# Kernel tuning notes

Hardware: AMD Instinct MI355X
Metric: run time of the kernel (lower is better)

Reference implementation:

```python
import jax, jax.numpy as jnp
import numpy as np
import math

N_EMBD = 1024
N_HEAD = 16
N_LAYER = 12


def setup_inputs() -> dict:
    key = jax.random.key(0)
    kx, kw, kb = jax.random.split(key, 3)
    B, T, C = 4, 2048, N_EMBD
    x = jax.random.normal(kx, (B, T, C), dtype=jnp.float32)
    # nn.Linear(C, 3C): weight [3C, C] scaled by 1/sqrt(2*n_layer), bias [3C]
    bound = 1.0 / math.sqrt(C)
    W = jax.random.uniform(kw, (3 * C, C), minval=-bound, maxval=bound, dtype=jnp.float32)
    W = W * (1.0 / math.sqrt(N_LAYER * 2))
    b = jax.random.uniform(kb, (3 * C,), minval=-bound, maxval=bound, dtype=jnp.float32)
    return {"x": x, "W": W, "b": b}


def reference(x, W, b) -> jnp.ndarray:
    B, T, C = x.shape
    H = N_HEAD
    D = C // H
    qkv = jnp.einsum("btc,oc->bto", x, W) + b  # [B, T, 3C]
    q, k, v = jnp.split(qkv, 3, axis=-1)
    # [B, H, T, D]
    q = q.reshape(B, T, H, D).transpose(0, 2, 1, 3)
    k = k.reshape(B, T, H, D).transpose(0, 2, 1, 3)
    v = v.reshape(B, T, H, D).transpose(0, 2, 1, 3)
    att = jnp.einsum("bhtd,bhsd->bhts", q, k) / math.sqrt(D)  # [B, H, T, T]
    causal = jnp.tril(jnp.ones((T, T), dtype=bool))
    att = jnp.where(causal, att, -jnp.inf)
    att = jax.nn.softmax(att, axis=-1)
    y = jnp.einsum("bhts,bhsd->bhtd", att, v)  # [B, H, T, D]
    return y.transpose(0, 2, 1, 3).reshape(B, T, C)
```

## Files before the change

kernel.cpp:

```cpp
#include <hip/hip_runtime.h>


typedef __attribute__((ext_vector_type(8))) short short8;
typedef __attribute__((ext_vector_type(4))) float f32x4;
typedef __attribute__((ext_vector_type(2))) int int2v;

#define AS1 __attribute__((address_space(1)))
#define AS3 __attribute__((address_space(3)))

__device__ __forceinline__ unsigned short f2bf(float f) {
  unsigned int u = __float_as_uint(f);
  u += 0x7fffu + ((u >> 16) & 1u);
  return (unsigned short)(u >> 16);
}

__device__ __forceinline__ unsigned int pack_bf16(float lo, float hi) {
  return __builtin_amdgcn_perm(__float_as_uint(hi) + 0x8000u,
                               __float_as_uint(lo) + 0x8000u, 0x07060302u);
}

__device__ __forceinline__ void async_copy16(const unsigned short* g, unsigned short* l) {
  const AS1 unsigned char* gp = (const AS1 unsigned char*)(unsigned long long)(uintptr_t)g;
  AS3 unsigned char* lp = (AS3 unsigned char*)(unsigned int)(uintptr_t)l;
  __builtin_amdgcn_global_load_lds((const AS1 void*)gp, (AS3 void*)lp, 16, 0, 0);
}

__global__ __launch_bounds__(256) void cvt_both(const float* __restrict__ x,
                                                const float* __restrict__ W,
                                                unsigned short* __restrict__ xt,
                                                unsigned short* __restrict__ wt) {
  int U = blockIdx.x * 256 + threadIdx.x;
  const float* in;
  unsigned short* out;
  if (U < 1048576) { in = x; out = xt; }
  else             { in = W; out = wt; U -= 1048576; }
  int u6 = U & 63, frag = (U >> 6) & 15, kt = (U >> 10) & 15, bt = U >> 14;
  int ks = frag & 1, i = (frag >> 1) & 3, half = frag >> 3;
  int row = bt * 128 + half * 64 + i * 16 + (u6 & 15);
  int colf = kt * 64 + ks * 32 + (u6 >> 4) * 8;
  const float4* p = (const float4*)(in + (size_t)row * 1024 + colf);
  float4 a = p[0], b = p[1];
  uint4 o;
  o.x = pack_bf16(a.x, a.y);
  o.y = pack_bf16(a.z, a.w);
  o.z = pack_bf16(b.x, b.y);
  o.w = pack_bf16(b.z, b.w);
  *(uint4*)(out + (size_t)U * 8) = o;
}

__global__ __launch_bounds__(256) void qkv_gemm(const unsigned short* __restrict__ xt,
                                                const unsigned short* __restrict__ wt,
                                                const float* __restrict__ bias,
                                                unsigned short* __restrict__ qb,
                                                unsigned short* __restrict__ kvb) {
  __shared__ unsigned short As[3][4096];
  __shared__ unsigned short Bs[3][4096];
  int tid = threadIdx.x;
  int wave = tid >> 6, lane = tid & 63;
  int q4 = lane >> 4, l16 = lane & 15;
  int bm = blockIdx.x, bn = blockIdx.y;

  f32x4 zero = {0.f, 0.f, 0.f, 0.f};
  f32x4 acc[4][4];
#pragma unroll
  for (int i = 0; i < 4; ++i)
#pragma unroll
    for (int j = 0; j < 4; ++j) acc[i][j] = zero;

  const unsigned short* Abase = xt + (size_t)bm * 16 * 8192;
  const unsigned short* Bbase = wt + (size_t)bn * 16 * 8192;

  auto stage = [&](int d, int kt32) {
    int kt64 = kt32 >> 1, ks = kt32 & 1;
    const unsigned short* ga = Abase + (size_t)kt64 * 8192;
    const unsigned short* gb = Bbase + (size_t)kt64 * 8192;
#pragma unroll
    for (int j = 0; j < 2; ++j) {
      int fi = wave * 2 + j;
      int f = (fi >> 2) * 8 + (fi & 3) * 2 + ks;
      async_copy16(ga + f * 512 + lane * 8, &As[d][fi * 512]);
      async_copy16(gb + f * 512 + lane * 8, &Bs[d][fi * 512]);
    }
  };

  auto compute = [&](const unsigned short* Ac, const unsigned short* Bc) {
    short8 af[4], bf[4];
#pragma unroll
    for (int i = 0; i < 4; ++i)
      af[i] = *(const short8*)(Ac + ((wave & 1) * 4 + i) * 512 + lane * 8);
#pragma unroll
    for (int j = 0; j < 4; ++j)
      bf[j] = *(const short8*)(Bc + ((wave >> 1) * 4 + j) * 512 + lane * 8);
#pragma unroll
    for (int i = 0; i < 4; ++i)
#pragma unroll
      for (int j = 0; j < 4; ++j)
        acc[i][j] = __builtin_amdgcn_mfma_f32_16x16x32_bf16(af[i], bf[j], acc[i][j], 0, 0, 0);
  };

  stage(0, 0);
  stage(1, 1);
  int cur = 0, nxt2 = 2;
  for (int kt = 0; kt < 31; ++kt) {
    asm volatile("s_waitcnt vmcnt(4)\n\ts_barrier" ::: "memory");
    if (kt < 30) stage(nxt2, kt + 2);
    compute(As[cur], Bs[cur]);
    cur = cur == 2 ? 0 : cur + 1;
    nxt2 = nxt2 == 2 ? 0 : nxt2 + 1;
  }
  asm volatile("s_waitcnt vmcnt(0)\n\ts_barrier" ::: "memory");
  compute(As[cur], Bs[cur]);

  const float QSCALE = 0.18033688011112042f;
  int rowbase = bm * 128 + (wave & 1) * 64;
  int colbase = bn * 128 + (wave >> 1) * 64;
#pragma unroll
  for (int j = 0; j < 4; ++j) {
    int o = colbase + j * 16 + l16;
    float bv = bias[o];
#pragma unroll
    for (int i = 0; i < 4; ++i) {
      int r0 = rowbase + i * 16 + q4 * 4;
      int b = r0 >> 11, t0 = r0 & 2047;
      if (o < 1024) {
        int h = o >> 6, d = o & 63;
#pragma unroll
        for (int r = 0; r < 4; ++r)
          qb[((((size_t)b * 16 + h) * 2048 + t0 + r) << 6) + d] =
              f2bf((acc[i][j][r] + bv) * QSCALE);
      } else if (o < 2048) {
        int o2 = o - 1024;
        int h = o2 >> 6, dd = o2 & 63;
        int st = t0 >> 6, s6 = t0 & 63;
        int ns = s6 >> 4, l16p = s6 & 15;
        int ks = dd >> 5, q4p = (dd & 31) >> 3, jj = dd & 7;
        size_t base = ((size_t)(b * 16 + h) * 32 + st) * 8192 +
                      ((ns * 2 + ks) * 64 + q4p * 16 + l16p) * 8 + jj;
#pragma unroll
        for (int r = 0; r < 4; ++r)
          kvb[base + r * 8] = f2bf(acc[i][j][r] + bv);
      } else {
        int o3 = o - 2048;
        int h = o3 >> 6, dd = o3 & 63;
        int st = t0 >> 6, s6 = t0 & 63;
        int a = s6 >> 5, q4p = (s6 >> 3) & 3, j0 = s6 & 7;
        int nd = dd >> 4, l16p = dd & 15;
        size_t base = ((size_t)(b * 16 + h) * 32 + st) * 8192 + 4096 +
                      (size_t)(((a * 4 + nd) * 64 + q4p * 16 + l16p) * 8 + j0);
        ushort4 pk;
        pk.x = f2bf(acc[i][j][0] + bv);
        pk.y = f2bf(acc[i][j][1] + bv);
        pk.z = f2bf(acc[i][j][2] + bv);
        pk.w = f2bf(acc[i][j][3] + bv);
        *(ushort4*)(&kvb[base]) = pk;
      }
    }
  }
}

__global__ __launch_bounds__(128, 3) void flash_attn(const unsigned short* __restrict__ qb,
                                                     const unsigned short* __restrict__ kvb,
                                                     float* __restrict__ out) {
  __shared__ unsigned short buf[2][8192];

  const int tid = threadIdx.x;
  const int wave = tid >> 6, lane = tid & 63;
  const int q4 = lane >> 4, l16 = lane & 15;
  const int n = blockIdx.x;
  const int bh = (n & 7) * 8 + ((n >> 3) & 7);
  const int bx = n >> 6;
  const int b = bh >> 4, h = bh & 15;

  const unsigned short* Qg = qb + (size_t)bh * (2048 * 64);
  const unsigned short* KVg = kvb + (size_t)bh * 32 * 8192;
  union { unsigned int u[4]; short8 s8; } ones_u;
  ones_u.u[0] = 0x3F803F80u; ones_u.u[1] = 0x3F803F80u;
  ones_u.u[2] = 0x3F803F80u; ones_u.u[3] = 0x3F803F80u;
  const short8 ones8 = ones_u.s8;

  auto stageK = [&](int d, int st) {
    const unsigned short* tp = KVg + (size_t)st * 8192;
#pragma unroll
    for (int i2 = 0; i2 < 4; ++i2) {
      int u = i2 * 128 + wave * 64;
      async_copy16(tp + (u + lane) * 8, &buf[d][u * 8]);
    }
  };
  auto stageV = [&](int d, int st) {
    const unsigned short* tp = KVg + (size_t)st * 8192 + 4096;
#pragma unroll
    for (int i2 = 0; i2 < 4; ++i2) {
      int u = i2 * 128 + wave * 64;
      async_copy16(tp + (u + lane) * 8, &buf[d][4096 + u * 8]);
    }
  };

  for (int pass = 0; pass < 2; ++pass) {
    const int qt = pass ? 31 - bx : bx;
    const int t0w = qt * 64 + wave * 32;

    short8 qf[2][2];
#pragma unroll
    for (int mt = 0; mt < 2; ++mt)
#pragma unroll
      for (int ks = 0; ks < 2; ++ks)
        qf[mt][ks] = *(const short8*)(Qg + (size_t)(t0w + mt * 16 + l16) * 64 +
                                      ks * 32 + q4 * 8);

    f32x4 zero = {0.f, 0.f, 0.f, 0.f};
    f32x4 oT[2][4];
#pragma unroll
    for (int mt = 0; mt < 2; ++mt)
#pragma unroll
      for (int nd = 0; nd < 4; ++nd) oT[mt][nd] = zero;
    f32x4 l_acc[2] = {zero, zero};
    short8 pf[2][2];

    auto qkt_build = [&](const unsigned short* kp, int tile) {
      f32x4 sT[2][4];
#pragma unroll
      for (int ns = 0; ns < 4; ++ns) {
        short8 kf0 = *(const short8*)(kp + (ns * 2 + 0) * 512 + lane * 8);
        short8 kf1 = *(const short8*)(kp + (ns * 2 + 1) * 512 + lane * 8);
#pragma unroll
        for (int mt = 0; mt < 2; ++mt) {
          sT[mt][ns] = __builtin_amdgcn_mfma_f32_16x16x32_bf16(kf0, qf[mt][0], zero, 0, 0, 0);
          sT[mt][ns] = __builtin_amdgcn_mfma_f32_16x16x32_bf16(kf1, qf[mt][1], sT[mt][ns], 0, 0, 0);
        }
      }
      if (tile == qt) {
#pragma unroll
        for (int mt = 0; mt < 2; ++mt) {
          int tg = t0w + mt * 16 + l16;
#pragma unroll
          for (int ns = 0; ns < 4; ++ns) {
            int sgb = qt * 64 + ns * 16 + q4 * 4;
#pragma unroll
            for (int r = 0; r < 4; ++r)
              if (sgb + r > tg) sT[mt][ns][r] = -3.0e38f;
          }
        }
      }
#pragma unroll
      for (int a = 0; a < 2; ++a)
#pragma unroll
        for (int mt = 0; mt < 2; ++mt) {
          unsigned int e0 = pack_bf16(__builtin_amdgcn_exp2f(sT[mt][2 * a][0]),
                                      __builtin_amdgcn_exp2f(sT[mt][2 * a][1]));
          unsigned int e1 = pack_bf16(__builtin_amdgcn_exp2f(sT[mt][2 * a][2]),
                                      __builtin_amdgcn_exp2f(sT[mt][2 * a][3]));
          unsigned int o0 = pack_bf16(__builtin_amdgcn_exp2f(sT[mt][2 * a + 1][0]),
                                      __builtin_amdgcn_exp2f(sT[mt][2 * a + 1][1]));
          unsigned int o1 = pack_bf16(__builtin_amdgcn_exp2f(sT[mt][2 * a + 1][2]),
                                      __builtin_amdgcn_exp2f(sT[mt][2 * a + 1][3]));
          int2v r0 = __builtin_amdgcn_permlane32_swap((int)e0, (int)o0, false, false);
          int2v r1 = __builtin_amdgcn_permlane32_swap((int)e1, (int)o1, false, false);
          int2v s0 = __builtin_amdgcn_permlane16_swap(r0.x, r0.y, false, false);
          int2v s1 = __builtin_amdgcn_permlane16_swap(r1.x, r1.y, false, false);
          union { int w[4]; short8 s8; } pu;
          pu.w[0] = s0.x;
          pu.w[1] = s1.x;
          pu.w[2] = s0.y;
          pu.w[3] = s1.y;
          pf[a][mt] = pu.s8;
        }
    };

    auto pv = [&](const unsigned short* vp) {
#pragma unroll
      for (int a = 0; a < 2; ++a) {
#pragma unroll
        for (int nd = 0; nd < 4; ++nd) {
          short8 vf = *(const short8*)(vp + ((a * 4 + nd) * 64 + lane) * 8);
#pragma unroll
          for (int mt = 0; mt < 2; ++mt)
            oT[mt][nd] = __builtin_amdgcn_mfma_f32_16x16x32_bf16(vf, pf[a][mt], oT[mt][nd], 0, 0, 0);
        }
#pragma unroll
        for (int mt = 0; mt < 2; ++mt)
          l_acc[mt] = __builtin_amdgcn_mfma_f32_16x16x32_bf16(ones8, pf[a][mt], l_acc[mt], 0, 0, 0);
      }
    };

    __syncthreads();
    stageK(0, 0);
    stageV(0, 0);
    if (qt >= 1) stageK(1, 1);
    __syncthreads();
    qkt_build(buf[0], 0);

    for (int st = 0; st < qt; ++st) {
      __syncthreads();
      if (st + 2 <= qt) stageK(st & 1, st + 2);
      stageV((st + 1) & 1, st + 1);
      __builtin_amdgcn_s_setprio(1);
      pv(buf[st & 1] + 4096);
      qkt_build(buf[(st + 1) & 1], st + 1);
      __builtin_amdgcn_s_setprio(0);
    }
    __syncthreads();
    __builtin_amdgcn_s_setprio(1);
    pv(buf[qt & 1] + 4096);
    __builtin_amdgcn_s_setprio(0);

#pragma unroll
    for (int mt = 0; mt < 2; ++mt) {
      float inv = 1.0f / l_acc[mt][0];
      int t = t0w + mt * 16 + l16;
      float* op = out + (size_t)(b * 2048 + t) * 1024 + h * 64 + q4 * 4;
#pragma unroll
      for (int nd = 0; nd < 4; ++nd) {
        float4 o4 = {oT[mt][nd][0] * inv, oT[mt][nd][1] * inv,
                     oT[mt][nd][2] * inv, oT[mt][nd][3] * inv};
        *(float4*)(op + nd * 16) = o4;
      }
    }
  }
}

extern "C" void kernel_launch(void* const* d_in, const int* in_sizes, int n_in,
                              void* d_out, int out_size, void* d_ws, size_t ws_size,
                              hipStream_t stream) {
  const float* x = (const float*)d_in[0];
  const float* W = (const float*)d_in[1];
  const float* bias = (const float*)d_in[2];
  float* out = (float*)d_out;

  char* ws = (char*)d_ws;
  unsigned short* xt = (unsigned short*)(ws);
  unsigned short* wt = (unsigned short*)(ws + 16777216);
  unsigned short* qb = (unsigned short*)(ws + 23068672);
  unsigned short* kvb = (unsigned short*)(ws + 39845888);

  hipLaunchKernelGGL(cvt_both, dim3(5632), dim3(256), 0, stream, x, W, xt, wt);
  hipLaunchKernelGGL(qkv_gemm, dim3(64, 24), dim3(256), 0, stream, xt, wt, bias,
                     qb, kvb);
  hipLaunchKernelGGL(flash_attn, dim3(1024), dim3(128), 0, stream, qb, kvb, out);
}
```

Measured before the change: 206.0 us.

## Use 4-wave blocks over 128-row query tiles, heaviest first; hardware bf16 pack

Flash attention moves from 2-wave blocks doing two balanced 64-row passes to 4-wave blocks that each own one 128-row query tile, sharing every staged K/V tile across twice as many waves. Blocks are issued longest-causal-range first instead of relying on the pass pairing for balance, and the diagonal mask now covers the two last key tiles. The bf16 packing of exponentials switches to the native v_cvt_pk_bf16_f32 instruction (round-to-nearest-even) instead of a perm-based add-and-truncate. The cost is per-block imbalance, now absorbed only by the scheduler, and a higher occupancy target on launch bounds that may constrain registers.

```diff
diff --git a/kernel.cpp b/kernel.cpp
--- a/kernel.cpp
+++ b/kernel.cpp
@@ -17,6 +17,12 @@
 __device__ __forceinline__ unsigned int pack_bf16(float lo, float hi) {
   return __builtin_amdgcn_perm(__float_as_uint(hi) + 0x8000u,
                                __float_as_uint(lo) + 0x8000u, 0x07060302u);
+}
+
+__device__ __forceinline__ unsigned int cvtpk(float lo, float hi) {
+  unsigned int r;
+  asm("v_cvt_pk_bf16_f32 %0, %1, %2" : "=v"(r) : "v"(lo), "v"(hi));
+  return r;
 }
 
 __device__ __forceinline__ void async_copy16(const unsigned short* g, unsigned short* l) {
@@ -158,7 +164,7 @@
   }
 }
 
-__global__ __launch_bounds__(128, 3) void flash_attn(const unsigned short* __restrict__ qb,
+__global__ __launch_bounds__(256, 5) void flash_attn(const unsigned short* __restrict__ qb,
                                                      const unsigned short* __restrict__ kvb,
                                                      float* __restrict__ out) {
   __shared__ unsigned short buf[2][8192];
@@ -168,8 +174,10 @@
   const int q4 = lane >> 4, l16 = lane & 15;
   const int n = blockIdx.x;
   const int bh = (n & 7) * 8 + ((n >> 3) & 7);
-  const int bx = n >> 6;
+  const int j = 15 - (n >> 6);
   const int b = bh >> 4, h = bh & 15;
+  const int stmax = 2 * j + 1;
+  const int t0w = j * 128 + wave * 32;
 
   const unsigned short* Qg = qb + (size_t)bh * (2048 * 64);
   const unsigned short* KVg = kvb + (size_t)bh * 32 * 8192;
@@ -181,139 +189,133 @@
   auto stageK = [&](int d, int st) {
     const unsigned short* tp = KVg + (size_t)st * 8192;
 #pragma unroll
-    for (int i2 = 0; i2 < 4; ++i2) {
-      int u = i2 * 128 + wave * 64;
+    for (int i2 = 0; i2 < 2; ++i2) {
+      int u = i2 * 256 + wave * 64;
       async_copy16(tp + (u + lane) * 8, &buf[d][u * 8]);
     }
   };
   auto stageV = [&](int d, int st) {
     const unsigned short* tp = KVg + (size_t)st * 8192 + 4096;
 #pragma unroll
-    for (int i2 = 0; i2 < 4; ++i2) {
-      int u = i2 * 128 + wave * 64;
+    for (int i2 = 0; i2 < 2; ++i2) {
+      int u = i2 * 256 + wave * 64;
       async_copy16(tp + (u + lane) * 8, &buf[d][4096 + u * 8]);
     }
   };
 
-  for (int pass = 0; pass < 2; ++pass) {
-    const int qt = pass ? 31 - bx : bx;
-    const int t0w = qt * 64 + wave * 32;
-
-    short8 qf[2][2];
-#pragma unroll
-    for (int mt = 0; mt < 2; ++mt)
-#pragma unroll
-      for (int ks = 0; ks < 2; ++ks)
-        qf[mt][ks] = *(const short8*)(Qg + (size_t)(t0w + mt * 16 + l16) * 64 +
-                                      ks * 32 + q4 * 8);
-
-    f32x4 zero = {0.f, 0.f, 0.f, 0.f};
-    f32x4 oT[2][4];
-#pragma unroll
-    for (int mt = 0; mt < 2; ++mt)
-#pragma unroll
-      for (int nd = 0; nd < 4; ++nd) oT[mt][nd] = zero;
-    f32x4 l_acc[2] = {zero, zero};
-    short8 pf[2][2];
-
-    auto qkt_build = [&](const unsigned short* kp, int tile) {
-      f32x4 sT[2][4];
-#pragma unroll
-      for (int ns = 0; ns < 4; ++ns) {
-        short8 kf0 = *(const short8*)(kp + (ns * 2 + 0) * 512 + lane * 8);
-        short8 kf1 = *(const short8*)(kp + (ns * 2 + 1) * 512 + lane * 8);
-#pragma unroll
-        for (int mt = 0; mt < 2; ++mt) {
-          sT[mt][ns] = __builtin_amdgcn_mfma_f32_16x16x32_bf16(kf0, qf[mt][0], zero, 0, 0, 0);
-          sT[mt][ns] = __builtin_amdgcn_mfma_f32_16x16x32_bf16(kf1, qf[mt][1], sT[mt][ns], 0, 0, 0);
+  short8 qf[2][2];
+#pragma unroll
+  for (int mt = 0; mt < 2; ++mt)
+#pragma unroll
+    for (int ks = 0; ks < 2; ++ks)
+      qf[mt][ks] = *(const short8*)(Qg + (size_t)(t0w + mt * 16 + l16) * 64 +
+                                    ks * 32 + q4 * 8);
+
+  f32x4 zero = {0.f, 0.f, 0.f, 0.f};
+  f32x4 oT[2][4];
+#pragma unroll
+  for (int mt = 0; mt < 2; ++mt)
+#pragma unroll
+    for (int nd = 0; nd < 4; ++nd) oT[mt][nd] = zero;
+  f32x4 l_acc[2] = {zero, zero};
+  short8 pf[2][2];
+
+  auto qkt_build = [&](const unsigned short* kp, int tile) {
+    f32x4 sT[2][4];
+#pragma unroll
+    for (int ns = 0; ns < 4; ++ns) {
+      short8 kf0 = *(const short8*)(kp + (ns * 2 + 0) * 512 + lane * 8);
+      short8 kf1 = *(const short8*)(kp + (ns * 2 + 1) * 512 + lane * 8);
+#pragma unroll
+      for (int mt = 0; mt < 2; ++mt) {
+        sT[mt][ns] = __builtin_amdgcn_mfma_f32_16x16x32_bf16(kf0, qf[mt][0], zero, 0, 0, 0);
+        sT[mt][ns] = __builtin_amdgcn_mfma_f32_16x16x32_bf16(kf1, qf[mt][1], sT[mt][ns], 0, 0, 0);
+      }
+    }
+    if (tile >= 2 * j) {
+#pragma unroll
+      for (int mt = 0; mt < 2; ++mt) {
+        int tg = t0w + mt * 16 + l16;
+#pragma unroll
+        for (int ns = 0; ns < 4; ++ns) {
+          int sgb = tile * 64 + ns * 16 + q4 * 4;
+#pragma unroll
+          for (int r = 0; r < 4; ++r)
+            if (sgb + r > tg) sT[mt][ns][r] = -3.0e38f;
         }
       }
-      if (tile == qt) {
-#pragma unroll
-        for (int mt = 0; mt < 2; ++mt) {
-          int tg = t0w + mt * 16 + l16;
-#pragma unroll
-          for (int ns = 0; ns < 4; ++ns) {
-            int sgb = qt * 64 + ns * 16 + q4 * 4;
-#pragma unroll
-            for (int r = 0; r < 4; ++r)
-              if (sgb + r > tg) sT[mt][ns][r] = -3.0e38f;
-          }
-        }
-      }
-#pragma unroll
-      for (int a = 0; a < 2; ++a)
-#pragma unroll
-        for (int mt = 0; mt < 2; ++mt) {
-          unsigned int e0 = pack_bf16(__builtin_amdgcn_exp2f(sT[mt][2 * a][0]),
-                                      __builtin_amdgcn_exp2f(sT[mt][2 * a][1]));
-          unsigned int e1 = pack_bf16(__builtin_amdgcn_exp2f(sT[mt][2 * a][2]),
-                                      __builtin_amdgcn_exp2f(sT[mt][2 * a][3]));
-          unsigned int o0 = pack_bf16(__builtin_amdgcn_exp2f(sT[mt][2 * a + 1][0]),
-                                      __builtin_amdgcn_exp2f(sT[mt][2 * a + 1][1]));
-          unsigned int o1 = pack_bf16(__builtin_amdgcn_exp2f(sT[mt][2 * a + 1][2]),
-                                      __builtin_amdgcn_exp2f(sT[mt][2 * a + 1][3]));
-          int2v r0 = __builtin_amdgcn_permlane32_swap((int)e0, (int)o0, false, false);
-          int2v r1 = __builtin_amdgcn_permlane32_swap((int)e1, (int)o1, false, false);
-          int2v s0 = __builtin_amdgcn_permlane16_swap(r0.x, r0.y, false, false);
-          int2v s1 = __builtin_amdgcn_permlane16_swap(r1.x, r1.y, false, false);
-          union { int w[4]; short8 s8; } pu;
-          pu.w[0] = s0.x;
-          pu.w[1] = s1.x;
-          pu.w[2] = s0.y;
-          pu.w[3] = s1.y;
-          pf[a][mt] = pu.s8;
-        }
-    };
-
-    auto pv = [&](const unsigned short* vp) {
-#pragma unroll
-      for (int a = 0; a < 2; ++a) {
-#pragma unroll
-        for (int nd = 0; nd < 4; ++nd) {
-          short8 vf = *(const short8*)(vp + ((a * 4 + nd) * 64 + lane) * 8);
-#pragma unroll
-          for (int mt = 0; mt < 2; ++mt)
-            oT[mt][nd] = __builtin_amdgcn_mfma_f32_16x16x32_bf16(vf, pf[a][mt], oT[mt][nd], 0, 0, 0);
-        }
+    }
+#pragma unroll
+    for (int a = 0; a < 2; ++a)
+#pragma unroll
+      for (int mt = 0; mt < 2; ++mt) {
+        unsigned int e0 = cvtpk(__builtin_amdgcn_exp2f(sT[mt][2 * a][0]),
+                                __builtin_amdgcn_exp2f(sT[mt][2 * a][1]));
+        unsigned int e1 = cvtpk(__builtin_amdgcn_exp2f(sT[mt][2 * a][2]),
+                                __builtin_amdgcn_exp2f(sT[mt][2 * a][3]));
+        unsigned int o0 = cvtpk(__builtin_amdgcn_exp2f(sT[mt][2 * a + 1][0]),
+                                __builtin_amdgcn_exp2f(sT[mt][2 * a + 1][1]));
+        unsigned int o1 = cvtpk(__builtin_amdgcn_exp2f(sT[mt][2 * a + 1][2]),
+                                __builtin_amdgcn_exp2f(sT[mt][2 * a + 1][3]));
+        int2v r0 = __builtin_amdgcn_permlane32_swap((int)e0, (int)o0, false, false);
+        int2v r1 = __builtin_amdgcn_permlane32_swap((int)e1, (int)o1, false, false);
+        int2v s0 = __builtin_amdgcn_permlane16_swap(r0.x, r0.y, false, false);
+        int2v s1 = __builtin_amdgcn_permlane16_swap(r1.x, r1.y, false, false);
+        union { int w[4]; short8 s8; } pu;
+        pu.w[0] = s0.x;
+        pu.w[1] = s1.x;
+        pu.w[2] = s0.y;
+        pu.w[3] = s1.y;
+        pf[a][mt] = pu.s8;
+      }
+  };
+
+  auto pv = [&](const unsigned short* vp) {
+#pragma unroll
+    for (int a = 0; a < 2; ++a) {
+#pragma unroll
+      for (int nd = 0; nd < 4; ++nd) {
+        short8 vf = *(const short8*)(vp + ((a * 4 + nd) * 64 + lane) * 8);
 #pragma unroll
         for (int mt = 0; mt < 2; ++mt)
-          l_acc[mt] = __builtin_amdgcn_mfma_f32_16x16x32_bf16(ones8, pf[a][mt], l_acc[mt], 0, 0, 0);
-      }
-    };
-
+          oT[mt][nd] = __builtin_amdgcn_mfma_f32_16x16x32_bf16(vf, pf[a][mt], oT[mt][nd], 0, 0, 0);
+      }
+#pragma unroll
+      for (int mt = 0; mt < 2; ++mt)
+        l_acc[mt] = __builtin_amdgcn_mfma_f32_16x16x32_bf16(ones8, pf[a][mt], l_acc[mt], 0, 0, 0);
+    }
+  };
+
+  stageK(0, 0);
+  stageV(0, 0);
+  stageK(1, 1);
+  __syncthreads();
+  qkt_build(buf[0], 0);
+
+  for (int st = 0; st < stmax; ++st) {
     __syncthreads();
-    stageK(0, 0);
-    stageV(0, 0);
-    if (qt >= 1) stageK(1, 1);
-    __syncthreads();
-    qkt_build(buf[0], 0);
-
-    for (int st = 0; st < qt; ++st) {
-      __syncthreads();
-      if (st + 2 <= qt) stageK(st & 1, st + 2);
-      stageV((st + 1) & 1, st + 1);
-      __builtin_amdgcn_s_setprio(1);
-      pv(buf[st & 1] + 4096);
-      qkt_build(buf[(st + 1) & 1], st + 1);
-      __builtin_amdgcn_s_setprio(0);
-    }
-    __syncthreads();
+    if (st + 2 <= stmax) stageK(st & 1, st + 2);
+    stageV((st + 1) & 1, st + 1);
     __builtin_amdgcn_s_setprio(1);
-    pv(buf[qt & 1] + 4096);
+    pv(buf[st & 1] + 4096);
+    qkt_build(buf[(st + 1) & 1], st + 1);
     __builtin_amdgcn_s_setprio(0);
-
-#pragma unroll
-    for (int mt = 0; mt < 2; ++mt) {
-      float inv = 1.0f / l_acc[mt][0];
-      int t = t0w + mt * 16 + l16;
-      float* op = out + (size_t)(b * 2048 + t) * 1024 + h * 64 + q4 * 4;
-#pragma unroll
-      for (int nd = 0; nd < 4; ++nd) {
-        float4 o4 = {oT[mt][nd][0] * inv, oT[mt][nd][1] * inv,
-                     oT[mt][nd][2] * inv, oT[mt][nd][3] * inv};
-        *(float4*)(op + nd * 16) = o4;
-      }
+  }
+  __syncthreads();
+  __builtin_amdgcn_s_setprio(1);
+  pv(buf[stmax & 1] + 4096);
+  __builtin_amdgcn_s_setprio(0);
+
+#pragma unroll
+  for (int mt = 0; mt < 2; ++mt) {
+    float inv = 1.0f / l_acc[mt][0];
+    int t = t0w + mt * 16 + l16;
+    float* op = out + (size_t)(b * 2048 + t) * 1024 + h * 64 + q4 * 4;
+#pragma unroll
+    for (int nd = 0; nd < 4; ++nd) {
+      float4 o4 = {oT[mt][nd][0] * inv, oT[mt][nd][1] * inv,
+                   oT[mt][nd][2] * inv, oT[mt][nd][3] * inv};
+      *(float4*)(op + nd * 16) = o4;
     }
   }
 }
@@ -335,5 +337,5 @@
   hipLaunchKernelGGL(cvt_both, dim3(5632), dim3(256), 0, stream, x, W, xt, wt);
   hipLaunchKernelGGL(qkv_gemm, dim3(64, 24), dim3(256), 0, stream, xt, wt, bias,
                      qb, kvb);
-  hipLaunchKernelGGL(flash_attn, dim3(1024), dim3(128), 0, stream, qb, kvb, out);
-}
+  hipLaunchKernelGGL(flash_attn, dim3(1024), dim3(256), 0, stream, qb, kvb, out);
+}
```

Result: slower. 269.5 us (+30.8%).
